# Performance work log

Measured on AMD Instinct MI355X. Metric: run time of the kernel, lower is better.

The kernel has to match this reference:

```python
import jax, jax.numpy as jnp
import numpy as np

NUM_VN = 4
HIDDEN = 64
N = 1_000_000
G = 8192


def setup_inputs() -> dict:
    key = jax.random.key(0)
    ks = jax.random.split(key, 8)
    node_feat = jax.random.normal(ks[0], (N, HIDDEN), dtype=jnp.float32)
    node_pos = jax.random.normal(ks[1], (N, 3), dtype=jnp.float32)
    vn_pos = jax.random.normal(ks[2], (G, 3 * NUM_VN), dtype=jnp.float32)
    batch = jnp.sort(jax.random.randint(ks[3], (N,), 0, G, dtype=jnp.int64))
    in_dim = NUM_VN ** 2  # 16
    s1 = 1.0 / np.sqrt(in_dim)
    s2 = 1.0 / np.sqrt(HIDDEN)
    W1 = jax.random.uniform(ks[4], (HIDDEN, in_dim), jnp.float32, -s1, s1)
    b1 = jax.random.uniform(ks[5], (HIDDEN,), jnp.float32, -s1, s1)
    W2 = jax.random.uniform(ks[6], (HIDDEN, HIDDEN), jnp.float32, -s2, s2)
    b2 = jax.random.uniform(ks[7], (HIDDEN,), jnp.float32, -s2, s2)
    return {"node_feat": node_feat, "node_pos": node_pos, "vn_pos": vn_pos,
            "batch": batch, "W1": W1, "b1": b1, "W2": W2, "b2": b2}


def _safe_cdist(v):
    # v: [N, num_vn, 3]; pairwise L2 distances -> [N, num_vn, num_vn]
    diff = v[:, :, None, :] - v[:, None, :, :]
    sq = jnp.sum(diff * diff, axis=-1)
    # sqrt with zero-safe gradient on the diagonal (matches torch.cdist grad=0 there)
    pos = sq > 0
    return jnp.where(pos, jnp.sqrt(jnp.where(pos, sq, 1.0)), 0.0)


def reference(node_feat, node_pos, vn_pos, batch, W1, b1, W2, b2):
    n = node_pos.shape[0]
    # gather per-node virtual-node positions, form relative vectors [N, num_vn, 3]
    info_vec = (jnp.tile(node_pos, (1, NUM_VN)) - vn_pos[batch]).reshape(n, NUM_VN, 3)
    info_scalar = _safe_cdist(info_vec).reshape(n, NUM_VN ** 2)
    norm = jnp.linalg.norm(info_scalar, axis=1, keepdims=True)
    info_scalar = info_scalar / (norm + 0.001)
    h = jax.nn.silu(info_scalar @ W1.T + b1)
    return h @ W2.T + b2
```

## Files before the change

### kernel.cpp

```cpp
#include <hip/hip_runtime.h>

#define LOG2E 1.44269504088896340736f

typedef __attribute__((ext_vector_type(8))) _Float16 half8;
typedef __attribute__((ext_vector_type(4))) float floatx4;

__global__ void prep_weights(const float* __restrict__ W1,
                             const float* __restrict__ W2,
                             float* __restrict__ W1e,
                             _Float16* __restrict__ W2h,
                             _Float16* __restrict__ W2l) {
    const int t = threadIdx.x;
    if (t < 64) {
        const int pa[6] = {0, 0, 0, 1, 1, 2};
        const int pb[6] = {1, 2, 3, 2, 3, 3};
#pragma unroll
        for (int p = 0; p < 6; ++p)
            W1e[t * 6 + p] = W1[t * 16 + pa[p] * 4 + pb[p]] + W1[t * 16 + pb[p] * 4 + pa[p]];
    }
#pragma unroll
    for (int e = t; e < 4096; e += 256) {
        const float f = W2[e];
        const _Float16 hi = (_Float16)f;
        W2h[e] = hi;
        W2l[e] = (_Float16)(f - (float)hi);
    }
}

__global__ __launch_bounds__(256, 4) void vnmlp_mfma(
    const float* __restrict__ node_pos,
    const float* __restrict__ vn_pos,
    const void*  __restrict__ batch_raw,
    const float* __restrict__ W1e,
    const _Float16* __restrict__ W2h,
    const _Float16* __restrict__ W2l,
    const float* __restrict__ b1,
    const float* __restrict__ b2,
    float*       __restrict__ out,
    int n)
{
    __shared__ _Float16 lds_h[256 * 64];

    const int t    = threadIdx.x;
    const int base = blockIdx.x * 256;
    const int i    = base + t;
    const bool valid = (i < n);

    float h[64];
    if (valid) {
        const int* b32 = (const int*)batch_raw;
        const int probe = b32[(n / 2) | 1] | b32[(n / 4) | 1] | b32[((n / 4) * 3) | 1];
        long long bi;
        if (probe == 0) bi = ((const long long*)batch_raw)[i];
        else            bi = (long long)b32[i];

        const float px = node_pos[3 * i + 0];
        const float py = node_pos[3 * i + 1];
        const float pz = node_pos[3 * i + 2];

        const float* vp = vn_pos + 12 * bi;
        float vx[4], vy[4], vz[4];
#pragma unroll
        for (int k = 0; k < 4; ++k) {
            vx[k] = px - vp[3 * k + 0];
            vy[k] = py - vp[3 * k + 1];
            vz[k] = pz - vp[3 * k + 2];
        }

        float dn[6];
        float ss = 0.0f;
        int p = 0;
#pragma unroll
        for (int a = 0; a < 4; ++a) {
#pragma unroll
            for (int k = a + 1; k < 4; ++k) {
                const float dx = vx[a] - vx[k];
                const float dy = vy[a] - vy[k];
                const float dz = vz[a] - vz[k];
                const float sq = dx * dx + dy * dy + dz * dz;
                dn[p++] = __builtin_amdgcn_sqrtf(sq);
                ss += sq;
            }
        }
        ss *= 2.0f;
        const float inv = __builtin_amdgcn_rcpf(__builtin_amdgcn_sqrtf(ss) + 0.001f);
#pragma unroll
        for (int q = 0; q < 6; ++q) dn[q] *= inv;

#pragma unroll
        for (int j = 0; j < 64; ++j) {
            float acc = b1[j];
#pragma unroll
            for (int q = 0; q < 6; ++q)
                acc = fmaf(dn[q], W1e[j * 6 + q], acc);
            const float e = __builtin_amdgcn_exp2f(-LOG2E * acc);
            h[j] = acc * __builtin_amdgcn_rcpf(1.0f + e);
        }
    } else {
#pragma unroll
        for (int j = 0; j < 64; ++j) h[j] = 0.0f;
    }

#pragma unroll
    for (int c = 0; c < 8; ++c) {
        half8 v;
#pragma unroll
        for (int j = 0; j < 8; ++j)
            v[j] = (_Float16)h[c * 8 + j];
        *(half8*)&lds_h[t * 64 + ((c ^ (t & 7)) * 8)] = v;
    }
    __syncthreads();

    const int l  = t & 63;
    const int w  = t >> 6;
    const int lm = l & 15;
    const int q  = l >> 4;

    half8 Bh[4][2], Bl[4][2];
#pragma unroll
    for (int c = 0; c < 4; ++c) {
#pragma unroll
        for (int ks = 0; ks < 2; ++ks) {
            const int off = (c * 16 + lm) * 64 + ks * 32 + q * 8;
            Bh[c][ks] = *(const half8*)(W2h + off);
            Bl[c][ks] = *(const half8*)(W2l + off);
        }
    }
    float bv[4];
#pragma unroll
    for (int c = 0; c < 4; ++c) bv[c] = b2[c * 16 + lm];

#pragma unroll 1
    for (int s = 0; s < 4; ++s) {
        const int nn = w * 64 + s * 16 + lm;
        half8 Ah[2];
#pragma unroll
        for (int ks = 0; ks < 2; ++ks) {
            const int kc = ks * 4 + q;
            Ah[ks] = *(const half8*)&lds_h[nn * 64 + ((kc ^ (nn & 7)) * 8)];
        }
#pragma unroll
        for (int c = 0; c < 4; ++c) {
            floatx4 acc;
            acc[0] = bv[c]; acc[1] = bv[c]; acc[2] = bv[c]; acc[3] = bv[c];
#pragma unroll
            for (int ks = 0; ks < 2; ++ks) {
                acc = __builtin_amdgcn_mfma_f32_16x16x32_f16(Ah[ks], Bh[c][ks], acc, 0, 0, 0);
                acc = __builtin_amdgcn_mfma_f32_16x16x32_f16(Ah[ks], Bl[c][ks], acc, 0, 0, 0);
            }
#pragma unroll
            for (int r = 0; r < 4; ++r) {
                const int node = base + w * 64 + s * 16 + q * 4 + r;
                if (node < n)
                    out[(size_t)node * 64 + c * 16 + lm] = acc[r];
            }
        }
    }
}

__global__ __launch_bounds__(256) void vnmlp_fallback(
    const float* __restrict__ node_pos, const float* __restrict__ vn_pos,
    const void* __restrict__ batch_raw, const float* __restrict__ W1,
    const float* __restrict__ b1, const float* __restrict__ W2,
    const float* __restrict__ b2, float* __restrict__ out, int n)
{
    __shared__ float lds[256 * 36];
    const int t = threadIdx.x;
    const int base = blockIdx.x * 256;
    const int i = base + t;
    const bool valid = (i < n);

    float h[64];
    if (valid) {
        const int* b32 = (const int*)batch_raw;
        const int probe = b32[(n / 2) | 1] | b32[(n / 4) | 1] | b32[((n / 4) * 3) | 1];
        long long bi;
        if (probe == 0) bi = ((const long long*)batch_raw)[i];
        else            bi = (long long)b32[i];
        const float px = node_pos[3 * i], py = node_pos[3 * i + 1], pz = node_pos[3 * i + 2];
        const float* vp = vn_pos + 12 * bi;
        float vx[4], vy[4], vz[4];
#pragma unroll
        for (int k = 0; k < 4; ++k) {
            vx[k] = px - vp[3 * k]; vy[k] = py - vp[3 * k + 1]; vz[k] = pz - vp[3 * k + 2];
        }
        float dn[6]; float ss = 0.0f; int p = 0;
#pragma unroll
        for (int a = 0; a < 4; ++a)
#pragma unroll
            for (int k = a + 1; k < 4; ++k) {
                const float dx = vx[a] - vx[k], dy = vy[a] - vy[k], dz = vz[a] - vz[k];
                const float sq = dx * dx + dy * dy + dz * dz;
                dn[p++] = __builtin_amdgcn_sqrtf(sq); ss += sq;
            }
        ss *= 2.0f;
        const float inv = __builtin_amdgcn_rcpf(__builtin_amdgcn_sqrtf(ss) + 0.001f);
#pragma unroll
        for (int qq = 0; qq < 6; ++qq) dn[qq] *= inv;
        const int pa[6] = {0, 0, 0, 1, 1, 2}, pb[6] = {1, 2, 3, 2, 3, 3};
#pragma unroll
        for (int j = 0; j < 64; ++j) {
            float acc = b1[j];
#pragma unroll
            for (int qq = 0; qq < 6; ++qq)
                acc = fmaf(dn[qq], W1[j * 16 + pa[qq] * 4 + pb[qq]] + W1[j * 16 + pb[qq] * 4 + pa[qq]], acc);
            const float e = __builtin_amdgcn_exp2f(-LOG2E * acc);
            h[j] = acc * __builtin_amdgcn_rcpf(1.0f + e);
        }
    }
    float4* o4 = (float4*)out;
#pragma unroll 1
    for (int half = 0; half < 2; ++half) {
        if (half) __syncthreads();
        if (valid) {
#pragma unroll 1
            for (int j4 = 0; j4 < 8; ++j4) {
                const int j0 = half * 32 + j4 * 4;
                float a0 = b2[j0], a1 = b2[j0 + 1], a2 = b2[j0 + 2], a3 = b2[j0 + 3];
#pragma unroll
                for (int k = 0; k < 64; ++k) {
                    const float hk = h[k];
                    a0 = fmaf(hk, W2[(j0 + 0) * 64 + k], a0);
                    a1 = fmaf(hk, W2[(j0 + 1) * 64 + k], a1);
                    a2 = fmaf(hk, W2[(j0 + 2) * 64 + k], a2);
                    a3 = fmaf(hk, W2[(j0 + 3) * 64 + k], a3);
                }
                *(float4*)&lds[t * 36 + j4 * 4] = make_float4(a0, a1, a2, a3);
            }
        }
        __syncthreads();
#pragma unroll
        for (int r = 0; r < 8; ++r) {
            const int g = r * 256 + t, node = g >> 3, sub = g & 7;
            if (base + node < n)
                o4[(size_t)(base + node) * 16 + half * 8 + sub] = *(const float4*)&lds[node * 36 + sub * 4];
        }
    }
}

extern "C" void kernel_launch(void* const* d_in, const int* in_sizes, int n_in,
                              void* d_out, int out_size, void* d_ws, size_t ws_size,
                              hipStream_t stream) {
    const float* node_pos = (const float*)d_in[1];
    const float* vn_pos   = (const float*)d_in[2];
    const void*  batch    = d_in[3];
    const float* W1       = (const float*)d_in[4];
    const float* b1       = (const float*)d_in[5];
    const float* W2       = (const float*)d_in[6];
    const float* b2       = (const float*)d_in[7];
    float* out = (float*)d_out;

    const int n = in_sizes[1] / 3;
    const int blocks = (n + 255) / 256;

    const size_t WS_NEED = 1536 + 8192 + 8192;
    if (ws_size >= WS_NEED) {
        float*    W1e = (float*)d_ws;
        _Float16* W2h = (_Float16*)((char*)d_ws + 1536);
        _Float16* W2l = (_Float16*)((char*)d_ws + 1536 + 8192);
        hipLaunchKernelGGL(prep_weights, dim3(1), dim3(256), 0, stream, W1, W2, W1e, W2h, W2l);
        hipLaunchKernelGGL(vnmlp_mfma, dim3(blocks), dim3(256), 0, stream,
                           node_pos, vn_pos, batch, W1e, W2h, W2l, b1, b2, out, n);
    } else {
        hipLaunchKernelGGL(vnmlp_fallback, dim3(blocks), dim3(256), 0, stream,
                           node_pos, vn_pos, batch, W1, b1, W2, b2, out, n);
    }
}
```

Before: 426.2 us.

## Drop block barrier, fuse hidden activation into LDS packing, hoist weight loads

Replaces the block-wide __syncthreads with a wave-local LDS wait. Each wave only reads the hidden rows its own lanes wrote, so no cross-wave barrier is needed. It also computes each SiLU output straight into its half8 LDS chunk instead of holding a 64-float array, which cuts register pressure. Three smaller changes ride along: the W2/b2 fragment loads are issued before the first-layer math to hide their latency, the virtual-node positions are read as float4, and out-of-range lanes are clamped so the per-thread branch and the per-row bounds check on stores disappear for full blocks. The barrier removal depends on the wave-local row mapping staying correct; if that mapping changes, it becomes a race.

```diff
diff --git a/kernel.cpp b/kernel.cpp
--- a/kernel.cpp
+++ b/kernel.cpp
@@ -44,31 +44,46 @@
     const int t    = threadIdx.x;
     const int base = blockIdx.x * 256;
     const int i    = base + t;
-    const bool valid = (i < n);
-
-    float h[64];
-    if (valid) {
-        const int* b32 = (const int*)batch_raw;
-        const int probe = b32[(n / 2) | 1] | b32[(n / 4) | 1] | b32[((n / 4) * 3) | 1];
-        long long bi;
-        if (probe == 0) bi = ((const long long*)batch_raw)[i];
-        else            bi = (long long)b32[i];
-
-        const float px = node_pos[3 * i + 0];
-        const float py = node_pos[3 * i + 1];
-        const float pz = node_pos[3 * i + 2];
-
-        const float* vp = vn_pos + 12 * bi;
-        float vx[4], vy[4], vz[4];
-#pragma unroll
-        for (int k = 0; k < 4; ++k) {
-            vx[k] = px - vp[3 * k + 0];
-            vy[k] = py - vp[3 * k + 1];
-            vz[k] = pz - vp[3 * k + 2];
-        }
-
-        float dn[6];
-        float ss = 0.0f;
+    const int ic   = (i < n) ? i : (n - 1);
+    const bool full = (base + 256 <= n);
+
+    const int l  = t & 63;
+    const int w  = t >> 6;
+    const int lm = l & 15;
+    const int q  = l >> 4;
+
+    half8 Bh[4][2], Bl[4][2];
+    float bv[4];
+#pragma unroll
+    for (int c = 0; c < 4; ++c) {
+#pragma unroll
+        for (int ks = 0; ks < 2; ++ks) {
+            const int off = (c * 16 + lm) * 64 + ks * 32 + q * 8;
+            Bh[c][ks] = *(const half8*)(W2h + off);
+            Bl[c][ks] = *(const half8*)(W2l + off);
+        }
+        bv[c] = b2[c * 16 + lm];
+    }
+
+    const int* b32 = (const int*)batch_raw;
+    const int probe = b32[(n / 2) | 1] | b32[(n / 4) | 1] | b32[((n / 4) * 3) | 1];
+    long long bi;
+    if (probe == 0) bi = ((const long long*)batch_raw)[ic];
+    else            bi = (long long)b32[ic];
+
+    const float px = node_pos[3 * ic + 0];
+    const float py = node_pos[3 * ic + 1];
+    const float pz = node_pos[3 * ic + 2];
+
+    const float4* vp4 = (const float4*)(vn_pos + 12 * bi);
+    const float4 v0 = vp4[0], v1 = vp4[1], v2 = vp4[2];
+    const float vx[4] = {px - v0.x, px - v0.w, px - v1.z, px - v2.y};
+    const float vy[4] = {py - v0.y, py - v1.x, py - v1.w, py - v2.z};
+    const float vz[4] = {pz - v0.z, pz - v1.y, pz - v2.x, pz - v2.w};
+
+    float dn[6];
+    float ss = 0.0f;
+    {
         int p = 0;
 #pragma unroll
         for (int a = 0; a < 4; ++a) {
@@ -82,53 +97,29 @@
                 ss += sq;
             }
         }
-        ss *= 2.0f;
-        const float inv = __builtin_amdgcn_rcpf(__builtin_amdgcn_sqrtf(ss) + 0.001f);
-#pragma unroll
-        for (int q = 0; q < 6; ++q) dn[q] *= inv;
-
-#pragma unroll
-        for (int j = 0; j < 64; ++j) {
-            float acc = b1[j];
-#pragma unroll
-            for (int q = 0; q < 6; ++q)
-                acc = fmaf(dn[q], W1e[j * 6 + q], acc);
-            const float e = __builtin_amdgcn_exp2f(-LOG2E * acc);
-            h[j] = acc * __builtin_amdgcn_rcpf(1.0f + e);
-        }
-    } else {
-#pragma unroll
-        for (int j = 0; j < 64; ++j) h[j] = 0.0f;
-    }
+    }
+    ss *= 2.0f;
+    const float inv = __builtin_amdgcn_rcpf(__builtin_amdgcn_sqrtf(ss) + 0.001f);
+#pragma unroll
+    for (int p = 0; p < 6; ++p) dn[p] *= inv;
 
 #pragma unroll
     for (int c = 0; c < 8; ++c) {
         half8 v;
 #pragma unroll
-        for (int j = 0; j < 8; ++j)
-            v[j] = (_Float16)h[c * 8 + j];
+        for (int jj = 0; jj < 8; ++jj) {
+            const int j = c * 8 + jj;
+            float acc = b1[j];
+#pragma unroll
+            for (int p = 0; p < 6; ++p)
+                acc = fmaf(dn[p], W1e[j * 6 + p], acc);
+            const float e = __builtin_amdgcn_exp2f(-LOG2E * acc);
+            v[jj] = (_Float16)(acc * __builtin_amdgcn_rcpf(1.0f + e));
+        }
         *(half8*)&lds_h[t * 64 + ((c ^ (t & 7)) * 8)] = v;
     }
-    __syncthreads();
-
-    const int l  = t & 63;
-    const int w  = t >> 6;
-    const int lm = l & 15;
-    const int q  = l >> 4;
-
-    half8 Bh[4][2], Bl[4][2];
-#pragma unroll
-    for (int c = 0; c < 4; ++c) {
-#pragma unroll
-        for (int ks = 0; ks < 2; ++ks) {
-            const int off = (c * 16 + lm) * 64 + ks * 32 + q * 8;
-            Bh[c][ks] = *(const half8*)(W2h + off);
-            Bl[c][ks] = *(const half8*)(W2l + off);
-        }
-    }
-    float bv[4];
-#pragma unroll
-    for (int c = 0; c < 4; ++c) bv[c] = b2[c * 16 + lm];
+
+    __asm__ volatile("s_waitcnt lgkmcnt(0)" ::: "memory");
 
 #pragma unroll 1
     for (int s = 0; s < 4; ++s) {
@@ -148,11 +139,17 @@
                 acc = __builtin_amdgcn_mfma_f32_16x16x32_f16(Ah[ks], Bh[c][ks], acc, 0, 0, 0);
                 acc = __builtin_amdgcn_mfma_f32_16x16x32_f16(Ah[ks], Bl[c][ks], acc, 0, 0, 0);
             }
-#pragma unroll
-            for (int r = 0; r < 4; ++r) {
-                const int node = base + w * 64 + s * 16 + q * 4 + r;
-                if (node < n)
-                    out[(size_t)node * 64 + c * 16 + lm] = acc[r];
+            if (full) {
+#pragma unroll
+                for (int r = 0; r < 4; ++r)
+                    out[(size_t)(base + w * 64 + s * 16 + q * 4 + r) * 64 + c * 16 + lm] = acc[r];
+            } else {
+#pragma unroll
+                for (int r = 0; r < 4; ++r) {
+                    const int node = base + w * 64 + s * 16 + q * 4 + r;
+                    if (node < n)
+                        out[(size_t)node * 64 + c * 16 + lm] = acc[r];
+                }
             }
         }
     }
```

After: 425.7 us. Within noise of the previous version (-0.1%).
